# Optimization experiments

Measured on AMD Instinct MI355X. Metric: run time of the kernel, lower is better.

Reference implementation:

```python
import jax, jax.numpy as jnp
import numpy as np

NUM_HEADS = 4
NUM_GROUPS = 8
EPS = 1e-5


def group_norm(x, w, b):
    # x: (B, C, H, W); normalize per group of C//NUM_GROUPS channels
    B, C, H, W = x.shape
    xg = x.reshape(B, NUM_GROUPS, C // NUM_GROUPS, H, W)
    mean = xg.mean(axis=(2, 3, 4), keepdims=True)
    var = xg.var(axis=(2, 3, 4), keepdims=True)
    xn = ((xg - mean) * jax.lax.rsqrt(var + EPS)).reshape(B, C, H, W)
    return xn * w[None, :, None, None] + b[None, :, None, None]


def conv1x1(x, w, b):
    # x: (B, C_in, H, W), w: (C_out, C_in), b: (C_out,)
    return jnp.einsum('bchw,oc->bohw', x, w) + b[None, :, None, None]


def setup_inputs() -> dict:
    key = jax.random.key(0)
    B, C, H, W = 4, 256, 64, 64
    k1, k2, k3 = jax.random.split(key, 3)
    scale = 1.0 / np.sqrt(C)
    return {
        'x': jax.random.normal(k1, (B, C, H, W), dtype=jnp.float32),
        'norm_w': jnp.ones((C,), dtype=jnp.float32),
        'norm_b': jnp.zeros((C,), dtype=jnp.float32),
        'qkv_w': jax.random.normal(k2, (3 * C, C), dtype=jnp.float32) * scale,
        'qkv_b': jnp.zeros((3 * C,), dtype=jnp.float32),
        'proj_w': jax.random.normal(k3, (C, C), dtype=jnp.float32) * scale,
        'proj_b': jnp.zeros((C,), dtype=jnp.float32),
    }


def reference(x, norm_w, norm_b, qkv_w, qkv_b, proj_w, proj_b):
    B, C, H, W = x.shape
    hd = C // NUM_HEADS  # head dim
    h = group_norm(x, norm_w, norm_b)
    qkv = conv1x1(h, qkv_w, qkv_b)            # (B, 3C, H, W)
    q, k, v = jnp.split(qkv, 3, axis=1)
    q = q.reshape(B, NUM_HEADS, hd, H * W)
    k = k.reshape(B, NUM_HEADS, hd, H * W)
    v = v.reshape(B, NUM_HEADS, hd, H * W)
    attn = jnp.einsum('bhcn,bhcm->bhnm', q, k) / jnp.sqrt(jnp.asarray(hd, x.dtype))
    attn = jax.nn.softmax(attn, axis=-1)
    out = jnp.einsum('bhnm,bhcm->bhcn', attn, v).reshape(B, C, H, W)
    out = conv1x1(out, proj_w, proj_b)
    return x + out
```

## Files before the change

### kernel.cpp

```cpp
#include <hip/hip_runtime.h>
#include <hip/hip_bf16.h>
#include <stdint.h>


#define B_  4
#define C_  256
#define N_  4096
#define NH_ 4
#define HD_ 64
#define G_  8
#define CPG_ 32
#define GRP_ELEMS (CPG_ * N_)

typedef __attribute__((ext_vector_type(8))) short short8;
typedef __attribute__((ext_vector_type(4))) float f32x4;
typedef __attribute__((ext_vector_type(4))) unsigned short us4;

__device__ __forceinline__ unsigned short f2bf(float f) {
  union { float f; unsigned u; } v; v.f = f;
  unsigned r = v.u + 0x7FFFu + ((v.u >> 16) & 1u);
  return (unsigned short)(r >> 16);
}

__device__ __forceinline__ unsigned pkbf2(float a, float b) {
  __hip_bfloat162 h = __float22bfloat162_rn(make_float2(a, b));
  unsigned r; __builtin_memcpy(&r, &h, sizeof(r)); return r;
}

__device__ __forceinline__ void dma16(const unsigned short* g, unsigned short* l) {
  __builtin_amdgcn_global_load_lds(
      (const __attribute__((address_space(1))) unsigned int*)(g),
      (__attribute__((address_space(3))) unsigned int*)(l), 16, 0, 0);
}

__global__ void cvt_weights(const float* __restrict__ qkvw,
                            const float* __restrict__ projw,
                            unsigned short* __restrict__ wq,
                            unsigned short* __restrict__ wp) {
  int i = blockIdx.x * 256 + threadIdx.x;
  if (i < 768 * 256) wq[i] = f2bf(qkvw[i]);
  if (i < 256 * 256) wp[i] = f2bf(projw[i]);
}

__global__ void gn_partial(const float* __restrict__ x, float* __restrict__ partial) {
  int idx = blockIdx.x;
  int slice = idx & 15, g = (idx >> 4) & 7, b = idx >> 7;
  int t = threadIdx.x;
  const float* base = x + (size_t)(b * C_ + g * CPG_) * N_ + slice * 256;
  float s = 0.f, sq = 0.f;
#pragma unroll
  for (int cc = 0; cc < CPG_; cc++) {
    float v = base[(size_t)cc * N_ + t];
    s += v; sq += v * v;
  }
#pragma unroll
  for (int off = 32; off; off >>= 1) {
    s  += __shfl_down(s,  off, 64);
    sq += __shfl_down(sq, off, 64);
  }
  __shared__ float ls[8];
  int wave = t >> 6, lane = t & 63;
  if (lane == 0) { ls[wave * 2] = s; ls[wave * 2 + 1] = sq; }
  __syncthreads();
  if (t == 0) {
    float S = ls[0] + ls[2] + ls[4] + ls[6];
    float SQ = ls[1] + ls[3] + ls[5] + ls[7];
    partial[idx * 2] = S; partial[idx * 2 + 1] = SQ;
  }
}

__global__ void gn_finalize(const float* __restrict__ partial, float* __restrict__ stats) {
  int t = threadIdx.x;
  if (t < 32) {
    float s = 0.f, sq = 0.f;
    for (int i = 0; i < 16; i++) {
      s  += partial[(t * 16 + i) * 2];
      sq += partial[(t * 16 + i) * 2 + 1];
    }
    const float inv = 1.0f / (float)GRP_ELEMS;
    float mean = s * inv;
    float var = sq * inv - mean * mean;
    stats[t * 2] = mean;
    stats[t * 2 + 1] = rsqrtf(var + 1e-5f);
  }
}

__global__ void gn_apply(const float* __restrict__ x,
                         const float* __restrict__ nw, const float* __restrict__ nb,
                         const float* __restrict__ stats, unsigned short* __restrict__ hT) {
  int nt = blockIdx.x, ct = blockIdx.y, b = blockIdx.z;
  __shared__ unsigned short tile[32][72];
  int t = threadIdx.x;
  int n_loc = t & 63, c_loc = t >> 6;
  float mean = stats[(b * G_ + ct) * 2];
  float rstd = stats[(b * G_ + ct) * 2 + 1];
  const float* xb = x + (size_t)(b * C_ + ct * CPG_) * N_ + nt * 64;
#pragma unroll
  for (int rr = 0; rr < 8; rr++) {
    int cc = rr * 4 + c_loc;
    int c = ct * CPG_ + cc;
    float v = xb[(size_t)cc * N_ + n_loc];
    v = (v - mean) * rstd * nw[c] + nb[c];
    tile[cc][n_loc] = f2bf(v);
  }
  __syncthreads();
  int c2 = t & 31, n2 = t >> 5;
  unsigned short* out = hT + ((size_t)(b * N_ + nt * 64)) * C_ + ct * CPG_ + c2;
#pragma unroll
  for (int pass = 0; pass < 8; pass++) {
    int n = pass * 8 + n2;
    out[(size_t)n * C_] = tile[c2][n];
  }
}

__global__ __launch_bounds__(256) void qkv_gemm(
    const unsigned short* __restrict__ hT, const unsigned short* __restrict__ wq,
    const float* __restrict__ qb,
    unsigned short* __restrict__ Qt, unsigned short* __restrict__ Kt,
    unsigned short* __restrict__ V) {
  int nt = blockIdx.x, ot = blockIdx.y, b = blockIdx.z;
  int t = threadIdx.x;
  int wave = t >> 6, lane = t & 63, l15 = lane & 15, quad = lane >> 4, l7 = l15 & 7;
  int o_base = ot * 64 + wave * 16;

  __shared__ __align__(16) unsigned short sh[64 * C_];
  {
    int row0 = wave * 2 + (lane >> 5);
    int col8 = lane & 31;
    int src8 = (col8 & 24) | ((col8 & 7) ^ (row0 & 7));
    const unsigned short* gsrc = hT + ((size_t)(b * N_ + nt * 64 + row0)) * C_ + src8 * 8;
#pragma unroll
    for (int it = 0; it < 8; it++)
      dma16(gsrc + (size_t)it * 8 * C_, sh + (it * 8 + wave * 2) * C_);
  }

  f32x4 acc[4];
#pragma unroll
  for (int tt = 0; tt < 4; tt++) acc[tt] = (f32x4){0.f, 0.f, 0.f, 0.f};

  const short8* arow = reinterpret_cast<const short8*>(wq + (size_t)(o_base + l15) * C_);

  asm volatile("s_waitcnt vmcnt(0)" ::: "memory");
  __syncthreads();

#pragma unroll
  for (int kk = 0; kk < 8; kk++) {
    short8 a = arow[kk * 4 + quad];
    int g = kk * 4 + quad;
    int col8 = (g & 24) | ((g & 7) ^ l7);
#pragma unroll
    for (int tt = 0; tt < 4; tt++) {
      short8 bf = *reinterpret_cast<const short8*>(&sh[(tt * 16 + l15) * C_ + col8 * 8]);
      acc[tt] = __builtin_amdgcn_mfma_f32_16x16x32_bf16(a, bf, acc[tt], 0, 0, 0);
    }
  }

  int sec = ot >> 2, head = ot & 3;
  int cw = wave * 16 + quad * 4;
  int bh = b * NH_ + head;
  const float SC = 0.125f * 1.44269504088896340736f;

  if (sec == 0) {
#pragma unroll
    for (int tt = 0; tt < 4; tt++) {
      int n = nt * 64 + tt * 16 + l15;
      us4 pk;
#pragma unroll
      for (int i = 0; i < 4; i++)
        pk[i] = f2bf((acc[tt][i] + qb[ot * 64 + cw + i]) * SC);
      *reinterpret_cast<us4*>(Qt + ((size_t)bh * N_ + n) * HD_ + cw) = pk;
    }
  } else if (sec == 1) {
#pragma unroll
    for (int tt = 0; tt < 4; tt++) {
      int n = nt * 64 + tt * 16 + l15;
      us4 pk;
#pragma unroll
      for (int i = 0; i < 4; i++)
        pk[i] = f2bf(acc[tt][i] + qb[ot * 64 + cw + i]);
      *reinterpret_cast<us4*>(Kt + ((size_t)bh * N_ + n) * HD_ + cw) = pk;
    }
  } else {
#pragma unroll
    for (int tt = 0; tt < 4; tt++) {
      int n = nt * 64 + tt * 16 + l15;
#pragma unroll
      for (int i = 0; i < 4; i++)
        V[((size_t)bh * HD_ + cw + i) * N_ + n] = f2bf(acc[tt][i] + qb[ot * 64 + cw + i]);
    }
  }
}

__global__ __launch_bounds__(256, 2) void flash_attn(
    const unsigned short* __restrict__ Qt, const unsigned short* __restrict__ Kt,
    const unsigned short* __restrict__ Vv, unsigned short* __restrict__ aoT) {
  int bh = blockIdx.x & 15, qt = blockIdx.x >> 4;
  int b = bh >> 2, head = bh & 3;
  int t = threadIdx.x;
  int wave = t >> 6, lane = t & 63, l15 = lane & 15, quad = lane >> 4;
  int l7 = l15 & 7;
  int qsub = wave >> 1, khalf = wave & 1;

  const unsigned short* Qb = Qt + (size_t)bh * N_ * HD_;
  const unsigned short* Kb = Kt + (size_t)bh * N_ * HD_;
  const unsigned short* Vb = Vv + (size_t)bh * HD_ * N_;
  int q_base = qt * 128 + qsub * 64;

  __shared__ __align__(16) unsigned char smem[72704];
  unsigned short* Pw = (unsigned short*)(smem + 65536 + wave * 1792);
  float* ObA = (float*)smem;
  float* ObB = (float*)(smem + 17408);
  float* lbA = (float*)(smem + 34816);
  float* lbB = (float*)(smem + 35072);

  const short8 vones = {(short)0x3F80, (short)0x3F80, (short)0x3F80, (short)0x3F80,
                        (short)0x3F80, (short)0x3F80, (short)0x3F80, (short)0x3F80};

  short8 qf[4][2];
#pragma unroll
  for (int r = 0; r < 4; r++)
#pragma unroll
    for (int h = 0; h < 2; h++)
      qf[r][h] = *reinterpret_cast<const short8*>(
          Qb + (size_t)(q_base + r * 16 + l15) * HD_ + h * 32 + quad * 8);

  f32x4 oa[4][4], la[4];
#pragma unroll
  for (int r = 0; r < 4; r++) {
    la[r] = (f32x4){0.f, 0.f, 0.f, 0.f};
#pragma unroll
    for (int ct = 0; ct < 4; ct++) oa[r][ct] = (f32x4){0.f, 0.f, 0.f, 0.f};
  }

  int i8 = lane >> 3, e8 = lane & 7;
  int r16 = lane >> 2, e4 = lane & 3;
  int kperm = (e8 ^ i8) * 8;
  int vperm = (e4 ^ ((r16 >> 1) & 3)) * 8;

  auto stage = [&](int kt2, int buf) {
    int m0 = khalf * 2048 + kt2 * 32;
    unsigned short* Kd = (unsigned short*)(smem + wave * 8192 + buf * 4096);
    unsigned short* Vd = (unsigned short*)(smem + 32768 + wave * 8192 + buf * 4096);
#pragma unroll
    for (int cc = 0; cc < 4; cc++) {
      dma16(Kb + (size_t)(m0 + cc * 8 + i8) * HD_ + kperm, Kd + cc * 512);
      dma16(Vb + (size_t)(cc * 16 + r16) * N_ + m0 + vperm, Vd + cc * 512);
    }
  };

  stage(0, 0);

#pragma unroll 1
  for (int kt = 0; kt < 64; kt++) {
    int buf = kt & 1;
    asm volatile("s_waitcnt vmcnt(0)" ::: "memory");
    if (kt + 1 < 64) stage(kt + 1, buf ^ 1);

    const unsigned short* Kw = (const unsigned short*)(smem + wave * 8192 + buf * 4096);
    const unsigned short* Vw = (const unsigned short*)(smem + 32768 + wave * 8192 + buf * 4096);

    short8 kf[2][2];
#pragma unroll
    for (int tt = 0; tt < 2; tt++)
#pragma unroll
      for (int kh = 0; kh < 2; kh++)
        kf[tt][kh] = *reinterpret_cast<const short8*>(
            &Kw[(tt * 16 + l15) * 64 + (((kh * 4 + quad) ^ l7) * 8)]);
    short8 vf[4];
#pragma unroll
    for (int ct = 0; ct < 4; ct++)
      vf[ct] = *reinterpret_cast<const short8*>(
          &Vw[(ct * 16 + l15) * 32 + ((quad ^ ((l15 >> 1) & 3)) * 8)]);

#pragma unroll
    for (int r = 0; r < 4; r++) {
      f32x4 s0, s1;
      {
        f32x4 z = (f32x4){0.f, 0.f, 0.f, 0.f};
        z  = __builtin_amdgcn_mfma_f32_16x16x32_bf16(kf[0][0], qf[r][0], z, 0, 0, 0);
        s0 = __builtin_amdgcn_mfma_f32_16x16x32_bf16(kf[0][1], qf[r][1], z, 0, 0, 0);
      }
      {
        f32x4 z = (f32x4){0.f, 0.f, 0.f, 0.f};
        z  = __builtin_amdgcn_mfma_f32_16x16x32_bf16(kf[1][0], qf[r][0], z, 0, 0, 0);
        s1 = __builtin_amdgcn_mfma_f32_16x16x32_bf16(kf[1][1], qf[r][1], z, 0, 0, 0);
      }
      union { unsigned u2[2]; us4 v; } w0, w1;
      w0.u2[0] = pkbf2(__builtin_amdgcn_exp2f(s0[0]), __builtin_amdgcn_exp2f(s0[1]));
      w0.u2[1] = pkbf2(__builtin_amdgcn_exp2f(s0[2]), __builtin_amdgcn_exp2f(s0[3]));
      w1.u2[0] = pkbf2(__builtin_amdgcn_exp2f(s1[0]), __builtin_amdgcn_exp2f(s1[1]));
      w1.u2[1] = pkbf2(__builtin_amdgcn_exp2f(s1[2]), __builtin_amdgcn_exp2f(s1[3]));
      *reinterpret_cast<us4*>(&Pw[l15 * 56 + quad * 4]) = w0.v;
      *reinterpret_cast<us4*>(&Pw[l15 * 56 + 16 + quad * 4]) = w1.v;
      short8 pf = *reinterpret_cast<const short8*>(&Pw[l15 * 56 + quad * 8]);
#pragma unroll
      for (int ct = 0; ct < 4; ct++)
        oa[r][ct] = __builtin_amdgcn_mfma_f32_16x16x32_bf16(vf[ct], pf, oa[r][ct], 0, 0, 0);
      la[r] = __builtin_amdgcn_mfma_f32_16x16x32_bf16(vones, pf, la[r], 0, 0, 0);
    }
  }

  __syncthreads();
  if (khalf == 1) {
    float* Ob = (qsub == 0) ? ObA : ObB;
    float* lb = (qsub == 0) ? lbA : lbB;
#pragma unroll
    for (int r = 0; r < 4; r++) {
#pragma unroll
      for (int ct = 0; ct < 4; ct++)
#pragma unroll
        for (int i = 0; i < 4; i++)
          Ob[(ct * 16 + quad * 4 + i) * 68 + r * 16 + l15] = oa[r][ct][i];
      if (quad == 0) lb[r * 16 + l15] = la[r][0];
    }
  }
  __syncthreads();
  if (khalf == 0) {
    const float* Ob = (qsub == 0) ? ObA : ObB;
    const float* lb = (qsub == 0) ? lbA : lbB;
#pragma unroll
    for (int r = 0; r < 4; r++) {
      float inv = 1.0f / (la[r][0] + lb[r * 16 + l15]);
      int n = q_base + r * 16 + l15;
#pragma unroll
      for (int ct = 0; ct < 4; ct++) {
        const float* ob = &Ob[(ct * 16 + quad * 4) * 68 + r * 16 + l15];
        union { unsigned u2[2]; us4 v; } w;
        w.u2[0] = pkbf2((oa[r][ct][0] + ob[0]) * inv, (oa[r][ct][1] + ob[68]) * inv);
        w.u2[1] = pkbf2((oa[r][ct][2] + ob[136]) * inv, (oa[r][ct][3] + ob[204]) * inv);
        *reinterpret_cast<us4*>(
            aoT + ((size_t)(b * N_ + n)) * C_ + head * HD_ + ct * 16 + quad * 4) = w.v;
      }
    }
  }
}

__global__ __launch_bounds__(256) void proj_gemm(
    const unsigned short* __restrict__ aoT, const unsigned short* __restrict__ wp,
    const float* __restrict__ pb, const float* __restrict__ x,
    float* __restrict__ out) {
  int nt = blockIdx.x, ot = blockIdx.y, b = blockIdx.z;
  int t = threadIdx.x;
  int wave = t >> 6, lane = t & 63, l15 = lane & 15, quad = lane >> 4, l7 = l15 & 7;
  int o_base = ot * 64 + wave * 16;

  __shared__ __align__(16) unsigned short sh[64 * C_];
  {
    int row0 = wave * 2 + (lane >> 5);
    int col8 = lane & 31;
    int src8 = (col8 & 24) | ((col8 & 7) ^ (row0 & 7));
    const unsigned short* gsrc = aoT + ((size_t)(b * N_ + nt * 64 + row0)) * C_ + src8 * 8;
#pragma unroll
    for (int it = 0; it < 8; it++)
      dma16(gsrc + (size_t)it * 8 * C_, sh + (it * 8 + wave * 2) * C_);
  }

  f32x4 acc[4];
#pragma unroll
  for (int tt = 0; tt < 4; tt++) acc[tt] = (f32x4){0.f, 0.f, 0.f, 0.f};

  const short8* arow = reinterpret_cast<const short8*>(wp + (size_t)(o_base + l15) * C_);

  asm volatile("s_waitcnt vmcnt(0)" ::: "memory");
  __syncthreads();

#pragma unroll
  for (int kk = 0; kk < 8; kk++) {
    short8 a = arow[kk * 4 + quad];
    int g = kk * 4 + quad;
    int col8 = (g & 24) | ((g & 7) ^ l7);
#pragma unroll
    for (int tt = 0; tt < 4; tt++) {
      short8 bf = *reinterpret_cast<const short8*>(&sh[(tt * 16 + l15) * C_ + col8 * 8]);
      acc[tt] = __builtin_amdgcn_mfma_f32_16x16x32_bf16(a, bf, acc[tt], 0, 0, 0);
    }
  }
#pragma unroll
  for (int tt = 0; tt < 4; tt++) {
    int n = nt * 64 + tt * 16 + l15;
#pragma unroll
    for (int i = 0; i < 4; i++) {
      int o = o_base + quad * 4 + i;
      size_t idx = ((size_t)(b * C_ + o)) * N_ + n;
      out[idx] = acc[tt][i] + pb[o] + x[idx];
    }
  }
}

extern "C" void kernel_launch(void* const* d_in, const int* in_sizes, int n_in,
                              void* d_out, int out_size, void* d_ws, size_t ws_size,
                              hipStream_t stream) {
  const float* x      = (const float*)d_in[0];
  const float* norm_w = (const float*)d_in[1];
  const float* norm_b = (const float*)d_in[2];
  const float* qkv_w  = (const float*)d_in[3];
  const float* qkv_b  = (const float*)d_in[4];
  const float* proj_w = (const float*)d_in[5];
  const float* proj_b = (const float*)d_in[6];
  float* out = (float*)d_out;

  char* ws = (char*)d_ws;
  size_t off = 0;
  auto alloc = [&](size_t bytes) { size_t o = off; off = (off + bytes + 255) & ~(size_t)255; return o; };
  size_t off_partial = alloc(512 * 2 * sizeof(float));
  size_t off_stats   = alloc(32 * 2 * sizeof(float));
  size_t off_wq      = alloc((size_t)768 * 256 * 2);
  size_t off_wp      = alloc((size_t)256 * 256 * 2);
  size_t off_hT      = alloc((size_t)B_ * N_ * C_ * 2);
  size_t off_Qt      = alloc((size_t)B_ * NH_ * N_ * HD_ * 2);
  size_t off_Kt      = alloc((size_t)B_ * NH_ * N_ * HD_ * 2);
  size_t off_V       = alloc((size_t)B_ * NH_ * HD_ * N_ * 2);
  size_t off_aoT     = alloc((size_t)B_ * N_ * C_ * 2);

  float* partial = (float*)(ws + off_partial);
  float* stats   = (float*)(ws + off_stats);
  unsigned short* wq  = (unsigned short*)(ws + off_wq);
  unsigned short* wp  = (unsigned short*)(ws + off_wp);
  unsigned short* hT  = (unsigned short*)(ws + off_hT);
  unsigned short* Qt  = (unsigned short*)(ws + off_Qt);
  unsigned short* Kt  = (unsigned short*)(ws + off_Kt);
  unsigned short* V   = (unsigned short*)(ws + off_V);
  unsigned short* aoT = (unsigned short*)(ws + off_aoT);

  cvt_weights<<<768, 256, 0, stream>>>(qkv_w, proj_w, wq, wp);
  gn_partial<<<512, 256, 0, stream>>>(x, partial);
  gn_finalize<<<1, 64, 0, stream>>>(partial, stats);
  gn_apply<<<dim3(64, 8, 4), 256, 0, stream>>>(x, norm_w, norm_b, stats, hT);
  qkv_gemm<<<dim3(64, 12, 4), 256, 0, stream>>>(hT, wq, qkv_b, Qt, Kt, V);
  flash_attn<<<512, 256, 0, stream>>>(Qt, Kt, V, aoT);
  proj_gemm<<<dim3(64, 4, 4), 256, 0, stream>>>(aoT, wp, proj_b, x, out);
}
```

Measured before the change: 209.5 us.

## Share K/V tiles across wave pairs and feed P via 16x16x16 MFMA

The two waves with the same key half now cooperatively stage a shared 64-key K/V tile with a barrier, instead of each wave staging its own 32-key tile. This halves global K/V traffic and doubles the work per iteration. The exp'd scores are fed straight from registers into 16x16x16 bf16 MFMAs, which removes the LDS round trip for P and shrinks shared memory. In exchange it adds a block-wide barrier every iteration and runs the PV product on a narrower MFMA shape, issuing more instructions.

```diff
diff --git a/kernel.cpp b/kernel.cpp
--- a/kernel.cpp
+++ b/kernel.cpp
@@ -13,6 +13,7 @@
 #define GRP_ELEMS (CPG_ * N_)
 
 typedef __attribute__((ext_vector_type(8))) short short8;
+typedef __attribute__((ext_vector_type(4))) short bf4;
 typedef __attribute__((ext_vector_type(4))) float f32x4;
 typedef __attribute__((ext_vector_type(4))) unsigned short us4;
 
@@ -206,15 +207,13 @@
   const unsigned short* Vb = Vv + (size_t)bh * HD_ * N_;
   int q_base = qt * 128 + qsub * 64;
 
-  __shared__ __align__(16) unsigned char smem[72704];
-  unsigned short* Pw = (unsigned short*)(smem + 65536 + wave * 1792);
+  __shared__ __align__(16) unsigned char smem[65536];
   float* ObA = (float*)smem;
   float* ObB = (float*)(smem + 17408);
   float* lbA = (float*)(smem + 34816);
   float* lbB = (float*)(smem + 35072);
 
-  const short8 vones = {(short)0x3F80, (short)0x3F80, (short)0x3F80, (short)0x3F80,
-                        (short)0x3F80, (short)0x3F80, (short)0x3F80, (short)0x3F80};
+  const bf4 vones4 = {(short)0x3F80, (short)0x3F80, (short)0x3F80, (short)0x3F80};
 
   short8 qf[4][2];
 #pragma unroll
@@ -233,70 +232,67 @@
   }
 
   int i8 = lane >> 3, e8 = lane & 7;
-  int r16 = lane >> 2, e4 = lane & 3;
-  int kperm = (e8 ^ i8) * 8;
-  int vperm = (e4 ^ ((r16 >> 1) & 3)) * 8;
-
+  int perm = (e8 ^ i8) * 8;
   auto stage = [&](int kt2, int buf) {
-    int m0 = khalf * 2048 + kt2 * 32;
-    unsigned short* Kd = (unsigned short*)(smem + wave * 8192 + buf * 4096);
-    unsigned short* Vd = (unsigned short*)(smem + 32768 + wave * 8192 + buf * 4096);
+    int m0 = khalf * 2048 + kt2 * 64;
+    unsigned short* Kd = (unsigned short*)(smem + khalf * 16384 + buf * 8192);
+    unsigned short* Vd = (unsigned short*)(smem + 32768 + khalf * 16384 + buf * 8192);
 #pragma unroll
     for (int cc = 0; cc < 4; cc++) {
-      dma16(Kb + (size_t)(m0 + cc * 8 + i8) * HD_ + kperm, Kd + cc * 512);
-      dma16(Vb + (size_t)(cc * 16 + r16) * N_ + m0 + vperm, Vd + cc * 512);
+      int c = qsub * 4 + cc;
+      dma16(Kb + (size_t)(m0 + c * 8 + i8) * HD_ + perm, Kd + c * 512);
+      dma16(Vb + (size_t)(c * 8 + i8) * N_ + m0 + perm, Vd + c * 512);
     }
   };
 
   stage(0, 0);
 
 #pragma unroll 1
-  for (int kt = 0; kt < 64; kt++) {
+  for (int kt = 0; kt < 32; kt++) {
     int buf = kt & 1;
     asm volatile("s_waitcnt vmcnt(0)" ::: "memory");
-    if (kt + 1 < 64) stage(kt + 1, buf ^ 1);
-
-    const unsigned short* Kw = (const unsigned short*)(smem + wave * 8192 + buf * 4096);
-    const unsigned short* Vw = (const unsigned short*)(smem + 32768 + wave * 8192 + buf * 4096);
-
-    short8 kf[2][2];
-#pragma unroll
-    for (int tt = 0; tt < 2; tt++)
+    __builtin_amdgcn_s_barrier();
+    if (kt + 1 < 32) stage(kt + 1, buf ^ 1);
+
+    const unsigned short* Kw = (const unsigned short*)(smem + khalf * 16384 + buf * 8192);
+    const unsigned short* Vw = (const unsigned short*)(smem + 32768 + khalf * 16384 + buf * 8192);
+
+    short8 kf[4][2];
+#pragma unroll
+    for (int tt = 0; tt < 4; tt++)
 #pragma unroll
       for (int kh = 0; kh < 2; kh++)
         kf[tt][kh] = *reinterpret_cast<const short8*>(
             &Kw[(tt * 16 + l15) * 64 + (((kh * 4 + quad) ^ l7) * 8)]);
-    short8 vf[4];
+
+    bf4 vf[4][4];
 #pragma unroll
     for (int ct = 0; ct < 4; ct++)
-      vf[ct] = *reinterpret_cast<const short8*>(
-          &Vw[(ct * 16 + l15) * 32 + ((quad ^ ((l15 >> 1) & 3)) * 8)]);
+#pragma unroll
+      for (int tt = 0; tt < 4; tt++)
+        vf[ct][tt] = *reinterpret_cast<const bf4*>(
+            &Vw[(ct * 16 + l15) * 64 + (((tt * 2 + (quad >> 1)) ^ l7) * 8) + (quad & 1) * 4]);
 
 #pragma unroll
     for (int r = 0; r < 4; r++) {
-      f32x4 s0, s1;
-      {
+      f32x4 s[4];
+#pragma unroll
+      for (int tt = 0; tt < 4; tt++) {
         f32x4 z = (f32x4){0.f, 0.f, 0.f, 0.f};
-        z  = __builtin_amdgcn_mfma_f32_16x16x32_bf16(kf[0][0], qf[r][0], z, 0, 0, 0);
-        s0 = __builtin_amdgcn_mfma_f32_16x16x32_bf16(kf[0][1], qf[r][1], z, 0, 0, 0);
+        z = __builtin_amdgcn_mfma_f32_16x16x32_bf16(kf[tt][0], qf[r][0], z, 0, 0, 0);
+        s[tt] = __builtin_amdgcn_mfma_f32_16x16x32_bf16(kf[tt][1], qf[r][1], z, 0, 0, 0);
       }
-      {
-        f32x4 z = (f32x4){0.f, 0.f, 0.f, 0.f};
-        z  = __builtin_amdgcn_mfma_f32_16x16x32_bf16(kf[1][0], qf[r][0], z, 0, 0, 0);
-        s1 = __builtin_amdgcn_mfma_f32_16x16x32_bf16(kf[1][1], qf[r][1], z, 0, 0, 0);
+#pragma unroll
+      for (int tt = 0; tt < 4; tt++) {
+        union { unsigned u2[2]; bf4 v; } w;
+        w.u2[0] = pkbf2(__builtin_amdgcn_exp2f(s[tt][0]), __builtin_amdgcn_exp2f(s[tt][1]));
+        w.u2[1] = pkbf2(__builtin_amdgcn_exp2f(s[tt][2]), __builtin_amdgcn_exp2f(s[tt][3]));
+        bf4 pf = w.v;
+#pragma unroll
+        for (int ct = 0; ct < 4; ct++)
+          oa[r][ct] = __builtin_amdgcn_mfma_f32_16x16x16bf16_1k(vf[ct][tt], pf, oa[r][ct], 0, 0, 0);
+        la[r] = __builtin_amdgcn_mfma_f32_16x16x16bf16_1k(vones4, pf, la[r], 0, 0, 0);
       }
-      union { unsigned u2[2]; us4 v; } w0, w1;
-      w0.u2[0] = pkbf2(__builtin_amdgcn_exp2f(s0[0]), __builtin_amdgcn_exp2f(s0[1]));
-      w0.u2[1] = pkbf2(__builtin_amdgcn_exp2f(s0[2]), __builtin_amdgcn_exp2f(s0[3]));
-      w1.u2[0] = pkbf2(__builtin_amdgcn_exp2f(s1[0]), __builtin_amdgcn_exp2f(s1[1]));
-      w1.u2[1] = pkbf2(__builtin_amdgcn_exp2f(s1[2]), __builtin_amdgcn_exp2f(s1[3]));
-      *reinterpret_cast<us4*>(&Pw[l15 * 56 + quad * 4]) = w0.v;
-      *reinterpret_cast<us4*>(&Pw[l15 * 56 + 16 + quad * 4]) = w1.v;
-      short8 pf = *reinterpret_cast<const short8*>(&Pw[l15 * 56 + quad * 8]);
-#pragma unroll
-      for (int ct = 0; ct < 4; ct++)
-        oa[r][ct] = __builtin_amdgcn_mfma_f32_16x16x32_bf16(vf[ct], pf, oa[r][ct], 0, 0, 0);
-      la[r] = __builtin_amdgcn_mfma_f32_16x16x32_bf16(vones, pf, la[r], 0, 0, 0);
     }
   }
 
```

After: 200.8 us. 1.04x faster.
